# Performance work log

Hardware: AMD Instinct MI355X
Metric: run time of the kernel (lower is better)

The kernel has to match this reference:

```python
import jax, jax.numpy as jnp
import numpy as np

N_DST = 50000
NUM_HEAD = 2
LN_EPS = 1e-5


def setup_inputs() -> dict:
    key = jax.random.key(0)
    ks = jax.random.split(key, 12)
    n_dst, n_src, E = 50000, 200000, 250000
    dim_node, dim_edge, dim_time, dim_out = 128, 64, 64, 128
    d_q = dim_node + dim_time            # w_q input dim
    d_k = dim_node + dim_edge + dim_time  # w_k / w_v input dim
    d_o = dim_node + dim_out              # w_out input dim
    f32 = jnp.float32
    return {
        "h": jax.random.normal(ks[0], (n_dst + n_src, dim_node), f32),
        "dt": jax.random.uniform(ks[1], (E,), f32) * 100.0,
        "ef": jax.random.normal(ks[2], (E, dim_edge), f32),
        # TimeEncode: cos(t * w + b), classic TGAT init w = 1/10^linspace(0,9)
        "time_w": (1.0 / 10.0 ** jnp.linspace(0.0, 9.0, dim_time)).astype(f32),
        "time_b": jnp.zeros((dim_time,), f32),
        "wq_w": (jax.random.normal(ks[3], (d_q, dim_out), f32) / np.sqrt(d_q)),
        "wq_b": jnp.zeros((dim_out,), f32),
        "wk_w": (jax.random.normal(ks[4], (d_k, dim_out), f32) / np.sqrt(d_k)),
        "wk_b": jnp.zeros((dim_out,), f32),
        "wv_w": (jax.random.normal(ks[5], (d_k, dim_out), f32) / np.sqrt(d_k)),
        "wv_b": jnp.zeros((dim_out,), f32),
        "wo_w": (jax.random.normal(ks[6], (d_o, dim_out), f32) / np.sqrt(d_o)),
        "wo_b": jnp.zeros((dim_out,), f32),
        "ln_g": jnp.ones((dim_out,), f32),
        "ln_b": jnp.zeros((dim_out,), f32),
        "nbr_idx": jax.random.randint(ks[7], (E,), 0, n_src),
        "edge_dst": jax.random.randint(ks[8], (E,), 0, n_dst),
    }


def reference(h, dt, ef, time_w, time_b, wq_w, wq_b, wk_w, wk_b, wv_w, wv_b,
              wo_w, wo_b, ln_g, ln_b, nbr_idx, edge_dst):
    n_dst = N_DST
    H = NUM_HEAD
    h_dst = h[:n_dst]                       # [n_dst, D]
    h_src = h[n_dst:]                       # [n_src, D]

    # time encoding: cos(t * w + b)
    time_feat = jnp.cos(dt[:, None] * time_w + time_b)          # [E, Dt]
    zero_time = jnp.broadcast_to(jnp.cos(time_b), (n_dst, time_b.shape[0]))

    Q_in = jnp.concatenate([h_dst, zero_time], axis=1)           # [n_dst, D+Dt]
    K_in = jnp.concatenate([h_src[nbr_idx], ef, time_feat], axis=1)  # [E, D+De+Dt]

    Q = (Q_in @ wq_w + wq_b)[edge_dst]      # [E, dim_out] gathered per edge
    K = K_in @ wk_w + wk_b                  # [E, dim_out]
    V = K_in @ wv_w + wv_b                  # [E, dim_out]

    E_ = Q.shape[0]
    Qh = Q.reshape(E_, H, -1)
    Kh = K.reshape(E_, H, -1)
    Vh = V.reshape(E_, H, -1)

    att_raw = jax.nn.leaky_relu(jnp.sum(Qh * Kh, axis=2), 0.2)   # [E, H]

    # edge_softmax: segment softmax over incoming edges of each dst node
    m = jax.ops.segment_max(att_raw, edge_dst, num_segments=n_dst)
    m = jnp.where(jnp.isfinite(m), m, 0.0)  # guard empty segments
    ex = jnp.exp(att_raw - m[edge_dst])
    den = jax.ops.segment_sum(ex, edge_dst, num_segments=n_dst)
    att = ex / den[edge_dst]                # [E, H]

    Vw = (Vh * att[..., None]).reshape(E_, -1)                   # [E, dim_out]
    agg = jax.ops.segment_sum(Vw, edge_dst, num_segments=n_dst)  # [n_dst, dim_out]

    pre = jax.nn.relu(jnp.concatenate([agg, h_dst], axis=1) @ wo_w + wo_b)
    mu = jnp.mean(pre, axis=-1, keepdims=True)
    var = jnp.var(pre, axis=-1, keepdims=True)
    return (pre - mu) / jnp.sqrt(var + LN_EPS) * ln_g + ln_b
```

## Files before the change

kernel.cpp:

```cpp
#include <hip/hip_runtime.h>
#include <hip/hip_bf16.h>
#include <math.h>


using bf16 = __hip_bfloat16;
typedef __attribute__((ext_vector_type(8))) short short8;
typedef __attribute__((ext_vector_type(4))) float f32x4;

static __device__ __forceinline__ unsigned short bf16_bits(float x) {
    bf16 h = __float2bfloat16(x);
    unsigned short b;
    __builtin_memcpy(&b, &h, 2);
    return b;
}
static __device__ __forceinline__ unsigned pk2(float x, float y) {
    return (unsigned)bf16_bits(x) | ((unsigned)bf16_bits(y) << 16);
}
static __device__ __forceinline__ float bflo(unsigned u) {
    return __uint_as_float(u << 16);
}
static __device__ __forceinline__ float bfhi(unsigned u) {
    return __uint_as_float(u & 0xffff0000u);
}
union frag_u { short8 s; unsigned u[4]; };

__global__ void k_pack(unsigned short* wkT, unsigned short* wvT, unsigned short* woT,
                       unsigned short* wqhT, unsigned short* wqlT, float* qbias,
                       const float* __restrict__ wk_w, const float* __restrict__ wv_w,
                       const float* __restrict__ wo_w, const float* __restrict__ wq_w,
                       const float* __restrict__ wq_b, const float* __restrict__ time_b) {
    int idx = blockIdx.x * blockDim.x + threadIdx.x;
    if (idx < 32768) {
        int n = idx >> 8, k = idx & 255;
        wkT[idx] = bf16_bits(wk_w[(size_t)k * 128 + n]);
        wvT[idx] = bf16_bits(wv_w[(size_t)k * 128 + n]);
        woT[idx] = bf16_bits(wo_w[(size_t)k * 128 + n]);
        if (idx < 16384) {
            int n2 = idx >> 7, k2 = idx & 127;
            float v = wq_w[(size_t)k2 * 128 + n2];
            unsigned short hb = bf16_bits(v);
            wqhT[idx] = hb;
            wqlT[idx] = bf16_bits(v - __uint_as_float((unsigned)hb << 16));
        }
        if (idx < 128) {
            float s = wq_b[idx];
            for (int j = 0; j < 64; ++j)
                s += cosf(time_b[j]) * wq_w[(128 + j) * 128 + idx];
            qbias[idx] = s;
        }
    }
}

__global__ void k_count(const int* __restrict__ edst, int* cnt, int E) {
    int e = blockIdx.x * 256 + threadIdx.x;
    if (e < E) atomicAdd(&cnt[edst[e]], 1);
}

__global__ void k_scan1(const int* __restrict__ cnt, int* rs, int* bsum, int n) {
    __shared__ int s[256];
    int t = threadIdx.x;
    int i = blockIdx.x * 256 + t;
    int v = (i < n) ? cnt[i] : 0;
    s[t] = v;
    __syncthreads();
    for (int off = 1; off < 256; off <<= 1) {
        int x = (t >= off) ? s[t - off] : 0;
        __syncthreads();
        s[t] += x;
        __syncthreads();
    }
    if (i < n) rs[i] = s[t] - v;
    if (t == 255) bsum[blockIdx.x] = s[255];
}

__global__ void k_scan2(int* bsum, int nblk) {
    __shared__ int s[256];
    int t = threadIdx.x;
    int v = (t < nblk) ? bsum[t] : 0;
    s[t] = v;
    __syncthreads();
    for (int off = 1; off < 256; off <<= 1) {
        int x = (t >= off) ? s[t - off] : 0;
        __syncthreads();
        s[t] += x;
        __syncthreads();
    }
    if (t < nblk) bsum[t] = s[t] - v;
}

__global__ void k_scatter(const int* __restrict__ edst, const int* __restrict__ rs,
                          const int* __restrict__ bsum, int* fill, int* epos, int E) {
    int e = blockIdx.x * 256 + threadIdx.x;
    if (e < E) {
        int d = edst[e];
        epos[e] = rs[d] + bsum[d >> 8] + atomicAdd(&fill[d], 1);
    }
}

__global__ __launch_bounds__(512) void k_q(
    float* __restrict__ Q, const float* __restrict__ h,
    const unsigned short* __restrict__ wqhT, const unsigned short* __restrict__ wqlT,
    const float* __restrict__ qbias, int ndst)
{
    __shared__ unsigned short Bs[32768];
    int tid = threadIdx.x;
    int lane = tid & 63, l15 = lane & 15, lk = lane >> 4;
    int r0 = blockIdx.x * 128 + (tid >> 6) * 16;
    int ra = r0 + l15;
    int rc = (ra < ndst) ? ra : (ndst - 1);
    const float* hrow = h + (size_t)rc * 128;

    float4 hx[4][2];
    #pragma unroll
    for (int kk = 0; kk < 4; ++kk) {
        int c0 = kk * 32 + lk * 8;
        hx[kk][0] = *reinterpret_cast<const float4*>(hrow + c0);
        hx[kk][1] = *reinterpret_cast<const float4*>(hrow + c0 + 4);
    }

    #pragma unroll
    for (int it = 0; it < 4; ++it) {
        int i = it * 512 + tid;
        int row = i >> 4, c = i & 15;
        int sw = row * 128 + ((c ^ (row & 15)) << 3);
        *reinterpret_cast<uint4*>(Bs + sw) =
            *reinterpret_cast<const uint4*>(wqhT + (size_t)row * 128 + c * 8);
        *reinterpret_cast<uint4*>(Bs + 16384 + sw) =
            *reinterpret_cast<const uint4*>(wqlT + (size_t)row * 128 + c * 8);
    }

    frag_u ah[4], al[4];
    #pragma unroll
    for (int kk = 0; kk < 4; ++kk) {
        float xs[8] = {hx[kk][0].x, hx[kk][0].y, hx[kk][0].z, hx[kk][0].w,
                       hx[kk][1].x, hx[kk][1].y, hx[kk][1].z, hx[kk][1].w};
        unsigned short hb[8];
        float lo[8];
        #pragma unroll
        for (int t = 0; t < 8; ++t) {
            hb[t] = bf16_bits(xs[t]);
            lo[t] = xs[t] - __uint_as_float((unsigned)hb[t] << 16);
        }
        #pragma unroll
        for (int t = 0; t < 4; ++t)
            ah[kk].u[t] = (unsigned)hb[2*t] | ((unsigned)hb[2*t+1] << 16);
        al[kk].u[0] = pk2(lo[0], lo[1]); al[kk].u[1] = pk2(lo[2], lo[3]);
        al[kk].u[2] = pk2(lo[4], lo[5]); al[kk].u[3] = pk2(lo[6], lo[7]);
    }

    f32x4 ck[8];
    #pragma unroll
    for (int nt = 0; nt < 8; ++nt) ck[nt] = (f32x4){0.f, 0.f, 0.f, 0.f};

    __syncthreads();
    #pragma unroll
    for (int kk2 = 0; kk2 < 4; ++kk2) {
        int co = ((kk2 * 4 + lk) ^ l15) << 3;
        #pragma unroll
        for (int nt = 0; nt < 8; ++nt) {
            int ro = (nt * 16 + l15) * 128;
            short8 bh = *reinterpret_cast<const short8*>(Bs + ro + co);
            short8 bl = *reinterpret_cast<const short8*>(Bs + 16384 + ro + co);
            ck[nt] = __builtin_amdgcn_mfma_f32_16x16x32_bf16(ah[kk2].s, bh, ck[nt], 0, 0, 0);
            ck[nt] = __builtin_amdgcn_mfma_f32_16x16x32_bf16(al[kk2].s, bh, ck[nt], 0, 0, 0);
            ck[nt] = __builtin_amdgcn_mfma_f32_16x16x32_bf16(ah[kk2].s, bl, ck[nt], 0, 0, 0);
        }
    }

    #pragma unroll
    for (int j = 0; j < 4; ++j) {
        int row = r0 + lk * 4 + j;
        if (row < ndst) {
            float4 qa = make_float4(ck[0][j] + qbias[0*16+l15], ck[1][j] + qbias[1*16+l15],
                                    ck[2][j] + qbias[2*16+l15], ck[3][j] + qbias[3*16+l15]);
            float4 qb = make_float4(ck[4][j] + qbias[4*16+l15], ck[5][j] + qbias[5*16+l15],
                                    ck[6][j] + qbias[6*16+l15], ck[7][j] + qbias[7*16+l15]);
            float* dst = Q + (size_t)row * 128 + l15 * 8;
            *reinterpret_cast<float4*>(dst)     = qa;
            *reinterpret_cast<float4*>(dst + 4) = qb;
        }
    }
}

__global__ __launch_bounds__(256) void k_kvA(
    const float* __restrict__ h, const int* __restrict__ nbr, const int* __restrict__ edst,
    const float* __restrict__ dt, const float* __restrict__ ef,
    const float* __restrict__ time_w, const float* __restrict__ time_b,
    const unsigned short* __restrict__ wkT, const unsigned short* __restrict__ wvT,
    const float* __restrict__ wk_b, const float* __restrict__ Q,
    const int* __restrict__ epos,
    unsigned short* __restrict__ Vbuf, float2* __restrict__ att2, int ndst, int E)
{
    __shared__ unsigned short Bs[16384];
    int tid  = threadIdx.x;
    int lane = tid & 63;
    int l15  = lane & 15;
    int lk   = lane >> 4;
    int e0   = blockIdx.x * 64 + (tid >> 6) * 16;

    int  ea = e0 + l15;
    bool va = ea < E;
    int  na = va ? nbr[ea] : 0;
    float da = va ? dt[ea] : 0.f;
    const float* hrow = h + (size_t)(ndst + na) * 128;
    const float* erow = ef + (size_t)ea * 64;

    int dstr[4], pe[4];
    bool evv[4];
    #pragma unroll
    for (int j = 0; j < 4; ++j) {
        int ed = e0 + lk * 4 + j;
        evv[j]  = ed < E;
        dstr[j] = evv[j] ? edst[ed] : 0;
        pe[j]   = evv[j] ? epos[ed] : 0;
    }

    float4 hx[4][2], ex_[2][2];
    const float4 z4 = make_float4(0.f, 0.f, 0.f, 0.f);
    #pragma unroll
    for (int kk = 0; kk < 4; ++kk) {
        int c0 = kk * 32 + lk * 8;
        hx[kk][0] = va ? *reinterpret_cast<const float4*>(hrow + c0)     : z4;
        hx[kk][1] = va ? *reinterpret_cast<const float4*>(hrow + c0 + 4) : z4;
    }
    #pragma unroll
    for (int t = 0; t < 2; ++t) {
        int c = (4 + t) * 32 + lk * 8 - 128;
        ex_[t][0] = va ? *reinterpret_cast<const float4*>(erow + c)     : z4;
        ex_[t][1] = va ? *reinterpret_cast<const float4*>(erow + c + 4) : z4;
    }

    float4 qa[4], qb[4];
    #pragma unroll
    for (int j = 0; j < 4; ++j) {
        const float* qp = Q + (size_t)dstr[j] * 128 + l15 * 8;
        qa[j] = *reinterpret_cast<const float4*>(qp);
        qb[j] = *reinterpret_cast<const float4*>(qp + 4);
    }

    #pragma unroll
    for (int it = 0; it < 8; ++it) {
        int i = it * 256 + tid;
        int row = i >> 4, c = i & 15;
        uint4 v = *reinterpret_cast<const uint4*>(wkT + (size_t)row * 256 + c * 8);
        *reinterpret_cast<uint4*>(Bs + row * 128 + ((c ^ (row & 15)) << 3)) = v;
    }

    float tf[16];
    {
        int j0 = lk * 8;
        #pragma unroll
        for (int t = 0; t < 8; ++t) tf[t]     = __cosf(fmaf(da, time_w[j0 + t],      time_b[j0 + t]));
        #pragma unroll
        for (int t = 0; t < 8; ++t) tf[8 + t] = __cosf(fmaf(da, time_w[j0 + 32 + t], time_b[j0 + 32 + t]));
    }

    frag_u a[8];
    #pragma unroll
    for (int kk = 0; kk < 4; ++kk) {
        a[kk].u[0] = pk2(hx[kk][0].x, hx[kk][0].y); a[kk].u[1] = pk2(hx[kk][0].z, hx[kk][0].w);
        a[kk].u[2] = pk2(hx[kk][1].x, hx[kk][1].y); a[kk].u[3] = pk2(hx[kk][1].z, hx[kk][1].w);
    }
    #pragma unroll
    for (int t = 0; t < 2; ++t) {
        a[4+t].u[0] = pk2(ex_[t][0].x, ex_[t][0].y); a[4+t].u[1] = pk2(ex_[t][0].z, ex_[t][0].w);
        a[4+t].u[2] = pk2(ex_[t][1].x, ex_[t][1].y); a[4+t].u[3] = pk2(ex_[t][1].z, ex_[t][1].w);
    }
    a[6].u[0] = pk2(tf[0], tf[1]);  a[6].u[1] = pk2(tf[2], tf[3]);
    a[6].u[2] = pk2(tf[4], tf[5]);  a[6].u[3] = pk2(tf[6], tf[7]);
    a[7].u[0] = pk2(tf[8], tf[9]);  a[7].u[1] = pk2(tf[10], tf[11]);
    a[7].u[2] = pk2(tf[12], tf[13]); a[7].u[3] = pk2(tf[14], tf[15]);

    f32x4 ck[8];
    #pragma unroll
    for (int nt = 0; nt < 8; ++nt) ck[nt] = (f32x4){0.f, 0.f, 0.f, 0.f};

    __syncthreads();
    #pragma unroll
    for (int kk2 = 0; kk2 < 4; ++kk2) {
        int co = ((kk2 * 4 + lk) ^ l15) << 3;
        #pragma unroll
        for (int nt = 0; nt < 8; ++nt) {
            short8 b = *reinterpret_cast<const short8*>(Bs + (nt * 16 + l15) * 128 + co);
            ck[nt] = __builtin_amdgcn_mfma_f32_16x16x32_bf16(a[kk2].s, b, ck[nt], 0, 0, 0);
        }
    }
    __syncthreads();
    #pragma unroll
    for (int it = 0; it < 8; ++it) {
        int i = it * 256 + tid;
        int row = i >> 4, c = i & 15;
        uint4 v = *reinterpret_cast<const uint4*>(wkT + (size_t)row * 256 + 128 + c * 8);
        *reinterpret_cast<uint4*>(Bs + row * 128 + ((c ^ (row & 15)) << 3)) = v;
    }
    __syncthreads();
    #pragma unroll
    for (int kk2 = 0; kk2 < 4; ++kk2) {
        int co = ((kk2 * 4 + lk) ^ l15) << 3;
        #pragma unroll
        for (int nt = 0; nt < 8; ++nt) {
            short8 b = *reinterpret_cast<const short8*>(Bs + (nt * 16 + l15) * 128 + co);
            ck[nt] = __builtin_amdgcn_mfma_f32_16x16x32_bf16(a[4 + kk2].s, b, ck[nt], 0, 0, 0);
        }
    }
    __syncthreads();
    #pragma unroll
    for (int it = 0; it < 8; ++it) {
        int i = it * 256 + tid;
        int row = i >> 4, c = i & 15;
        uint4 v = *reinterpret_cast<const uint4*>(wvT + (size_t)row * 256 + c * 8);
        *reinterpret_cast<uint4*>(Bs + row * 128 + ((c ^ (row & 15)) << 3)) = v;
    }

    float p0[4], p1[4];
    #pragma unroll
    for (int j = 0; j < 4; ++j) { p0[j] = 0.f; p1[j] = 0.f; }
    #pragma unroll
    for (int nt = 0; nt < 8; ++nt) {
        float kb = wk_b[nt * 16 + l15];
        #pragma unroll
        for (int j = 0; j < 4; ++j) {
            float qv = (nt < 4) ? ((const float*)&qa[j])[nt] : ((const float*)&qb[j])[nt - 4];
            float t = (ck[nt][j] + kb) * qv;
            if (nt < 4) p0[j] += t; else p1[j] += t;
        }
    }
    #pragma unroll
    for (int m = 1; m <= 8; m <<= 1)
        #pragma unroll
        for (int j = 0; j < 4; ++j) {
            p0[j] += __shfl_xor(p0[j], m, 64);
            p1[j] += __shfl_xor(p1[j], m, 64);
        }
    if (l15 == 0) {
        #pragma unroll
        for (int j = 0; j < 4; ++j)
            if (evv[j]) {
                float r0 = p0[j]; r0 = (r0 >= 0.f) ? r0 : 0.2f * r0;
                float r1 = p1[j]; r1 = (r1 >= 0.f) ? r1 : 0.2f * r1;
                att2[pe[j]] = make_float2(r0, r1);
            }
    }

    f32x4 cv[8];
    #pragma unroll
    for (int nt = 0; nt < 8; ++nt) cv[nt] = (f32x4){0.f, 0.f, 0.f, 0.f};
    __syncthreads();
    #pragma unroll
    for (int kk2 = 0; kk2 < 4; ++kk2) {
        int co = ((kk2 * 4 + lk) ^ l15) << 3;
        #pragma unroll
        for (int nt = 0; nt < 8; ++nt) {
            short8 b = *reinterpret_cast<const short8*>(Bs + (nt * 16 + l15) * 128 + co);
            cv[nt] = __builtin_amdgcn_mfma_f32_16x16x32_bf16(a[kk2].s, b, cv[nt], 0, 0, 0);
        }
    }
    __syncthreads();
    #pragma unroll
    for (int it = 0; it < 8; ++it) {
        int i = it * 256 + tid;
        int row = i >> 4, c = i & 15;
        uint4 v = *reinterpret_cast<const uint4*>(wvT + (size_t)row * 256 + 128 + c * 8);
        *reinterpret_cast<uint4*>(Bs + row * 128 + ((c ^ (row & 15)) << 3)) = v;
    }
    __syncthreads();
    #pragma unroll
    for (int kk2 = 0; kk2 < 4; ++kk2) {
        int co = ((kk2 * 4 + lk) ^ l15) << 3;
        #pragma unroll
        for (int nt = 0; nt < 8; ++nt) {
            short8 b = *reinterpret_cast<const short8*>(Bs + (nt * 16 + l15) * 128 + co);
            cv[nt] = __builtin_amdgcn_mfma_f32_16x16x32_bf16(a[4 + kk2].s, b, cv[nt], 0, 0, 0);
        }
    }

    #pragma unroll
    for (int j = 0; j < 4; ++j)
        if (evv[j]) {
            uint4 val;
            val.x = pk2(cv[0][j], cv[1][j]);
            val.y = pk2(cv[2][j], cv[3][j]);
            val.z = pk2(cv[4][j], cv[5][j]);
            val.w = pk2(cv[6][j], cv[7][j]);
            *reinterpret_cast<uint4*>(Vbuf + (size_t)pe[j] * 128 + l15 * 8) = val;
        }
}

__global__ __launch_bounds__(256) void k_agg(
    const unsigned short* __restrict__ Vbuf, const float2* __restrict__ att2,
    const int* __restrict__ rs, const int* __restrict__ bsum, const int* __restrict__ cnt,
    const float* __restrict__ wv_b, unsigned short* __restrict__ agg16, int ndst)
{
    int w = threadIdx.x >> 6, lane = threadIdx.x & 63;
    int d = blockIdx.x * 4 + w;
    if (d >= ndst) return;
    int p0 = lane * 2, p1 = p0 + 1;
    int c0 = ((p0 & 7) << 4) + (p0 >> 3);
    int c1 = ((p1 & 7) << 4) + (p1 >> 3);
    bool h0 = (p0 & 4) != 0, h1 = (p1 & 4) != 0;
    int base = rs[d] + bsum[d >> 8], n = cnt[d];
    const unsigned* V32 = reinterpret_cast<const unsigned*>(Vbuf);
    float den0 = 0.f, den1 = 0.f, acc0 = 0.f, acc1 = 0.f;
    int i = 0;
    for (; i + 4 <= n; i += 4) {
        size_t r = (size_t)(base + i);
        float2 a0 = att2[r], a1 = att2[r+1], a2 = att2[r+2], a3 = att2[r+3];
        unsigned w0 = V32[r*64 + lane], w1 = V32[(r+1)*64 + lane];
        unsigned w2 = V32[(r+2)*64 + lane], w3 = V32[(r+3)*64 + lane];
        float e00 = __expf(a0.x), e01 = __expf(a0.y);
        float e10 = __expf(a1.x), e11 = __expf(a1.y);
        float e20 = __expf(a2.x), e21 = __expf(a2.y);
        float e30 = __expf(a3.x), e31 = __expf(a3.y);
        den0 += e00 + e10 + e20 + e30;
        den1 += e01 + e11 + e21 + e31;
        acc0 = fmaf(h0 ? e01 : e00, bflo(w0), acc0);
        acc1 = fmaf(h1 ? e01 : e00, bfhi(w0), acc1);
        acc0 = fmaf(h0 ? e11 : e10, bflo(w1), acc0);
        acc1 = fmaf(h1 ? e11 : e10, bfhi(w1), acc1);
        acc0 = fmaf(h0 ? e21 : e20, bflo(w2), acc0);
        acc1 = fmaf(h1 ? e21 : e20, bfhi(w2), acc1);
        acc0 = fmaf(h0 ? e31 : e30, bflo(w3), acc0);
        acc1 = fmaf(h1 ? e31 : e30, bfhi(w3), acc1);
    }
    for (; i < n; ++i) {
        size_t r = (size_t)(base + i);
        float2 at = att2[r];
        float ex0 = __expf(at.x), ex1 = __expf(at.y);
        den0 += ex0; den1 += ex1;
        unsigned vv = V32[r*64 + lane];
        acc0 = fmaf(h0 ? ex1 : ex0, bflo(vv), acc0);
        acc1 = fmaf(h1 ? ex1 : ex0, bfhi(vv), acc1);
    }
    float o0 = 0.f, o1 = 0.f;
    if (n > 0) {
        o0 = acc0 / (h0 ? den1 : den0) + wv_b[c0];
        o1 = acc1 / (h1 ? den1 : den0) + wv_b[c1];
    }
    agg16[(size_t)d * 128 + c0] = bf16_bits(o0);
    agg16[(size_t)d * 128 + c1] = bf16_bits(o1);
}

__global__ __launch_bounds__(512) void k_out(
    const unsigned short* __restrict__ agg16, const float* __restrict__ h,
    const unsigned short* __restrict__ woT, const float* __restrict__ wo_b,
    const float* __restrict__ ln_g, const float* __restrict__ ln_b,
    float* __restrict__ out, int ndst)
{
    __shared__ unsigned short Bs[32768];
    int tid = threadIdx.x;
    int lane = tid & 63, l15 = lane & 15, lk = lane >> 4;
    int r0 = blockIdx.x * 128 + (tid >> 6) * 16;
    int ra = r0 + l15;
    int rc = (ra < ndst) ? ra : (ndst - 1);
    const unsigned short* arow = agg16 + (size_t)rc * 128;
    const float* hrow = h + (size_t)rc * 128;

    frag_u aa[4];
    float4 hx[4][2];
    #pragma unroll
    for (int kk = 0; kk < 4; ++kk) {
        int c0 = kk * 32 + lk * 8;
        aa[kk].s = *reinterpret_cast<const short8*>(arow + c0);
        hx[kk][0] = *reinterpret_cast<const float4*>(hrow + c0);
        hx[kk][1] = *reinterpret_cast<const float4*>(hrow + c0 + 4);
    }

    #pragma unroll
    for (int it = 0; it < 8; ++it) {
        int i = it * 512 + tid;
        int row = i >> 5, c = i & 31;
        uint4 v = *reinterpret_cast<const uint4*>(woT + (size_t)row * 256 + c * 8);
        *reinterpret_cast<uint4*>(Bs + row * 256 + ((c ^ (row & 15)) << 3)) = v;
    }

    frag_u ah[4];
    #pragma unroll
    for (int kk = 0; kk < 4; ++kk) {
        ah[kk].u[0] = pk2(hx[kk][0].x, hx[kk][0].y); ah[kk].u[1] = pk2(hx[kk][0].z, hx[kk][0].w);
        ah[kk].u[2] = pk2(hx[kk][1].x, hx[kk][1].y); ah[kk].u[3] = pk2(hx[kk][1].z, hx[kk][1].w);
    }

    f32x4 ck[8];
    #pragma unroll
    for (int nt = 0; nt < 8; ++nt) ck[nt] = (f32x4){0.f, 0.f, 0.f, 0.f};

    __syncthreads();
    #pragma unroll
    for (int kk2 = 0; kk2 < 4; ++kk2) {
        int coA = ((kk2 * 4 + lk) ^ l15) << 3;
        int coH = (((16 + kk2 * 4 + lk)) ^ l15) << 3;
        #pragma unroll
        for (int nt = 0; nt < 8; ++nt) {
            int ro = (nt * 16 + l15) * 256;
            short8 bA = *reinterpret_cast<const short8*>(Bs + ro + coA);
            short8 bH = *reinterpret_cast<const short8*>(Bs + ro + coH);
            ck[nt] = __builtin_amdgcn_mfma_f32_16x16x32_bf16(aa[kk2].s, bA, ck[nt], 0, 0, 0);
            ck[nt] = __builtin_amdgcn_mfma_f32_16x16x32_bf16(ah[kk2].s, bH, ck[nt], 0, 0, 0);
        }
    }

    #pragma unroll
    for (int nt = 0; nt < 8; ++nt) {
        float bo = wo_b[nt * 16 + l15];
        #pragma unroll
        for (int j = 0; j < 4; ++j)
            ck[nt][j] = fmaxf(ck[nt][j] + bo, 0.f);
    }
    float s1[4], s2[4];
    #pragma unroll
    for (int j = 0; j < 4; ++j) { s1[j] = 0.f; s2[j] = 0.f; }
    #pragma unroll
    for (int nt = 0; nt < 8; ++nt)
        #pragma unroll
        for (int j = 0; j < 4; ++j) {
            s1[j] += ck[nt][j];
            s2[j] = fmaf(ck[nt][j], ck[nt][j], s2[j]);
        }
    #pragma unroll
    for (int m = 1; m <= 8; m <<= 1)
        #pragma unroll
        for (int j = 0; j < 4; ++j) {
            s1[j] += __shfl_xor(s1[j], m, 64);
            s2[j] += __shfl_xor(s2[j], m, 64);
        }
    float mean[4], rstd[4];
    #pragma unroll
    for (int j = 0; j < 4; ++j) {
        mean[j] = s1[j] * (1.f / 128.f);
        float var = s2[j] * (1.f / 128.f) - mean[j] * mean[j];
        rstd[j] = rsqrtf(var + 1e-5f);
    }
    #pragma unroll
    for (int nt = 0; nt < 8; ++nt) {
        int col = nt * 16 + l15;
        float g = ln_g[col], lb = ln_b[col];
        #pragma unroll
        for (int j = 0; j < 4; ++j) {
            int row = r0 + lk * 4 + j;
            if (row < ndst)
                out[(size_t)row * 128 + col] = (ck[nt][j] - mean[j]) * rstd[j] * g + lb;
        }
    }
}

extern "C" void kernel_launch(void* const* d_in, const int* in_sizes, int n_in,
                              void* d_out, int out_size, void* d_ws, size_t ws_size,
                              hipStream_t stream) {
    const float* h      = (const float*)d_in[0];
    const float* dt     = (const float*)d_in[1];
    const float* ef     = (const float*)d_in[2];
    const float* time_w = (const float*)d_in[3];
    const float* time_b = (const float*)d_in[4];
    const float* wq_w   = (const float*)d_in[5];
    const float* wq_b   = (const float*)d_in[6];
    const float* wk_w   = (const float*)d_in[7];
    const float* wk_b   = (const float*)d_in[8];
    const float* wv_w   = (const float*)d_in[9];
    const float* wv_b   = (const float*)d_in[10];
    const float* wo_w   = (const float*)d_in[11];
    const float* wo_b   = (const float*)d_in[12];
    const float* ln_g   = (const float*)d_in[13];
    const float* ln_b   = (const float*)d_in[14];
    const int* nbr      = (const int*)d_in[15];
    const int* edst     = (const int*)d_in[16];

    int E    = in_sizes[1];
    int ndst = out_size / 128;
    int nblk = (ndst + 255) / 256;

    char* wsb = (char*)d_ws;
    float* qbias = (float*)wsb;                 wsb += 512;
    float* Q     = (float*)wsb;                 wsb += (size_t)ndst * 128 * 4;
    unsigned short* agg16 = (unsigned short*)wsb; wsb += (size_t)ndst * 128 * 2;
    unsigned short* wkT  = (unsigned short*)wsb; wsb += 32768 * 2;
    unsigned short* wvT  = (unsigned short*)wsb; wsb += 32768 * 2;
    unsigned short* woT  = (unsigned short*)wsb; wsb += 32768 * 2;
    unsigned short* wqhT = (unsigned short*)wsb; wsb += 16384 * 2;
    unsigned short* wqlT = (unsigned short*)wsb; wsb += 16384 * 2;
    int* cnt    = (int*)wsb;                    wsb += (size_t)ndst * 4;
    int* fill   = (int*)wsb;                    wsb += (size_t)ndst * 4;
    int* rs     = (int*)wsb;                    wsb += (size_t)ndst * 4;
    int* bsum   = (int*)wsb;                    wsb += 1024;
    int* epos   = (int*)wsb;                    wsb += (size_t)E * 4;
    float2* att2 = (float2*)wsb;                wsb += (size_t)E * 8;
    unsigned short* Vbuf = (unsigned short*)wsb; wsb += (size_t)E * 128 * 2;

    hipMemsetAsync(cnt, 0, (size_t)ndst * 8, stream);
    k_pack<<<128, 256, 0, stream>>>(wkT, wvT, woT, wqhT, wqlT, qbias,
                                    wk_w, wv_w, wo_w, wq_w, wq_b, time_b);
    k_count<<<(E + 255) / 256, 256, 0, stream>>>(edst, cnt, E);
    k_scan1<<<nblk, 256, 0, stream>>>(cnt, rs, bsum, ndst);
    k_scan2<<<1, 256, 0, stream>>>(bsum, nblk);
    k_scatter<<<(E + 255) / 256, 256, 0, stream>>>(edst, rs, bsum, fill, epos, E);
    k_q<<<(ndst + 127) / 128, 512, 0, stream>>>(Q, h, wqhT, wqlT, qbias, ndst);
    k_kvA<<<(E + 63) / 64, 256, 0, stream>>>(h, nbr, edst, dt, ef, time_w, time_b,
                                             wkT, wvT, wk_b, Q, epos, Vbuf, att2, ndst, E);
    k_agg<<<(ndst + 3) / 4, 256, 0, stream>>>(Vbuf, att2, rs, bsum, cnt, wv_b, agg16, ndst);
    k_out<<<(ndst + 127) / 128, 512, 0, stream>>>(agg16, h, woT, wo_b, ln_g, ln_b,
                                                  (float*)d_out, ndst);
}
```

Measured before the change: 229.7 us.

## Double-buffer K/V weight staging in shared memory across quarter-K chunks

Splits the K and V weight loads into 64-column quarters and ping-pongs them between two shared-memory buffers, so the next quarter is staged while MFMAs run on the current one. The aim is to hide global-to-LDS weight load latency behind compute and to cut the number of barriers that serialize loading and math. Total LDS stays at 32 KB, and the XOR swizzle changes to an 8-wide pattern to match the narrower rows. Correctness depends on the barrier placement between buffer reuse steps.

```diff
diff --git a/kernel.cpp b/kernel.cpp
--- a/kernel.cpp
+++ b/kernel.cpp
@@ -182,6 +182,36 @@
     }
 }
 
+#define STAGEQ(qq, bb)                                                              \
+    {                                                                               \
+        const unsigned short* _src = ((qq) < 4) ? wkT : wvT;                        \
+        const int _qk = (qq) & 3;                                                   \
+        _Pragma("unroll")                                                           \
+        for (int _it = 0; _it < 4; ++_it) {                                         \
+            int _i = _it * 256 + tid;                                               \
+            int _row = _i >> 3, _c = _i & 7;                                        \
+            uint4 _v = *reinterpret_cast<const uint4*>(                             \
+                _src + (size_t)_row * 256 + _qk * 64 + _c * 8);                     \
+            *reinterpret_cast<uint4*>(                                              \
+                &Bs[bb][_row * 64 + ((_c ^ (_row & 7)) << 3)]) = _v;                \
+        }                                                                           \
+    }
+
+#define GEMMQ(acc, abase, bb)                                                       \
+    {                                                                               \
+        _Pragma("unroll")                                                           \
+        for (int _kk2 = 0; _kk2 < 2; ++_kk2) {                                      \
+            _Pragma("unroll")                                                       \
+            for (int _nt = 0; _nt < 8; ++_nt) {                                     \
+                short8 _b = *reinterpret_cast<const short8*>(                       \
+                    &Bs[bb][(_nt * 16 + l15) * 64 +                                 \
+                            (((_kk2 * 4 + lk) ^ (l15 & 7)) << 3)]);                 \
+                acc[_nt] = __builtin_amdgcn_mfma_f32_16x16x32_bf16(                 \
+                    a[(abase) + _kk2].s, _b, acc[_nt], 0, 0, 0);                    \
+            }                                                                       \
+        }                                                                           \
+    }
+
 __global__ __launch_bounds__(256) void k_kvA(
     const float* __restrict__ h, const int* __restrict__ nbr, const int* __restrict__ edst,
     const float* __restrict__ dt, const float* __restrict__ ef,
@@ -191,7 +221,7 @@
     const int* __restrict__ epos,
     unsigned short* __restrict__ Vbuf, float2* __restrict__ att2, int ndst, int E)
 {
-    __shared__ unsigned short Bs[16384];
+    __shared__ unsigned short Bs[2][8192];
     int tid  = threadIdx.x;
     int lane = tid & 63;
     int l15  = lane & 15;
@@ -238,13 +268,7 @@
         qb[j] = *reinterpret_cast<const float4*>(qp + 4);
     }
 
-    #pragma unroll
-    for (int it = 0; it < 8; ++it) {
-        int i = it * 256 + tid;
-        int row = i >> 4, c = i & 15;
-        uint4 v = *reinterpret_cast<const uint4*>(wkT + (size_t)row * 256 + c * 8);
-        *reinterpret_cast<uint4*>(Bs + row * 128 + ((c ^ (row & 15)) << 3)) = v;
-    }
+    STAGEQ(0, 0);
 
     float tf[16];
     {
@@ -276,41 +300,10 @@
     for (int nt = 0; nt < 8; ++nt) ck[nt] = (f32x4){0.f, 0.f, 0.f, 0.f};
 
     __syncthreads();
-    #pragma unroll
-    for (int kk2 = 0; kk2 < 4; ++kk2) {
-        int co = ((kk2 * 4 + lk) ^ l15) << 3;
-        #pragma unroll
-        for (int nt = 0; nt < 8; ++nt) {
-            short8 b = *reinterpret_cast<const short8*>(Bs + (nt * 16 + l15) * 128 + co);
-            ck[nt] = __builtin_amdgcn_mfma_f32_16x16x32_bf16(a[kk2].s, b, ck[nt], 0, 0, 0);
-        }
-    }
-    __syncthreads();
-    #pragma unroll
-    for (int it = 0; it < 8; ++it) {
-        int i = it * 256 + tid;
-        int row = i >> 4, c = i & 15;
-        uint4 v = *reinterpret_cast<const uint4*>(wkT + (size_t)row * 256 + 128 + c * 8);
-        *reinterpret_cast<uint4*>(Bs + row * 128 + ((c ^ (row & 15)) << 3)) = v;
-    }
-    __syncthreads();
-    #pragma unroll
-    for (int kk2 = 0; kk2 < 4; ++kk2) {
-        int co = ((kk2 * 4 + lk) ^ l15) << 3;
-        #pragma unroll
-        for (int nt = 0; nt < 8; ++nt) {
-            short8 b = *reinterpret_cast<const short8*>(Bs + (nt * 16 + l15) * 128 + co);
-            ck[nt] = __builtin_amdgcn_mfma_f32_16x16x32_bf16(a[4 + kk2].s, b, ck[nt], 0, 0, 0);
-        }
-    }
-    __syncthreads();
-    #pragma unroll
-    for (int it = 0; it < 8; ++it) {
-        int i = it * 256 + tid;
-        int row = i >> 4, c = i & 15;
-        uint4 v = *reinterpret_cast<const uint4*>(wvT + (size_t)row * 256 + c * 8);
-        *reinterpret_cast<uint4*>(Bs + row * 128 + ((c ^ (row & 15)) << 3)) = v;
-    }
+    STAGEQ(1, 1); GEMMQ(ck, 0, 0); __syncthreads();
+    STAGEQ(2, 0); GEMMQ(ck, 2, 1); __syncthreads();
+    STAGEQ(3, 1); GEMMQ(ck, 4, 0); __syncthreads();
+    STAGEQ(4, 0); GEMMQ(ck, 6, 1);
 
     float p0[4], p1[4];
     #pragma unroll
@@ -341,38 +334,15 @@
                 att2[pe[j]] = make_float2(r0, r1);
             }
     }
+    __syncthreads();
 
     f32x4 cv[8];
     #pragma unroll
     for (int nt = 0; nt < 8; ++nt) cv[nt] = (f32x4){0.f, 0.f, 0.f, 0.f};
-    __syncthreads();
-    #pragma unroll
-    for (int kk2 = 0; kk2 < 4; ++kk2) {
-        int co = ((kk2 * 4 + lk) ^ l15) << 3;
-        #pragma unroll
-        for (int nt = 0; nt < 8; ++nt) {
-            short8 b = *reinterpret_cast<const short8*>(Bs + (nt * 16 + l15) * 128 + co);
-            cv[nt] = __builtin_amdgcn_mfma_f32_16x16x32_bf16(a[kk2].s, b, cv[nt], 0, 0, 0);
-        }
-    }
-    __syncthreads();
-    #pragma unroll
-    for (int it = 0; it < 8; ++it) {
-        int i = it * 256 + tid;
-        int row = i >> 4, c = i & 15;
-        uint4 v = *reinterpret_cast<const uint4*>(wvT + (size_t)row * 256 + 128 + c * 8);
-        *reinterpret_cast<uint4*>(Bs + row * 128 + ((c ^ (row & 15)) << 3)) = v;
-    }
-    __syncthreads();
-    #pragma unroll
-    for (int kk2 = 0; kk2 < 4; ++kk2) {
-        int co = ((kk2 * 4 + lk) ^ l15) << 3;
-        #pragma unroll
-        for (int nt = 0; nt < 8; ++nt) {
-            short8 b = *reinterpret_cast<const short8*>(Bs + (nt * 16 + l15) * 128 + co);
-            cv[nt] = __builtin_amdgcn_mfma_f32_16x16x32_bf16(a[4 + kk2].s, b, cv[nt], 0, 0, 0);
-        }
-    }
+    STAGEQ(5, 1); GEMMQ(cv, 0, 0); __syncthreads();
+    STAGEQ(6, 0); GEMMQ(cv, 2, 1); __syncthreads();
+    STAGEQ(7, 1); GEMMQ(cv, 4, 0); __syncthreads();
+    GEMMQ(cv, 6, 1);
 
     #pragma unroll
     for (int j = 0; j < 4; ++j)
```

New measurement: 235.8 us. +2.7%, slower.
